# Kernel optimization log

Hardware: AMD Instinct MI355X
Metric: run time of the kernel (lower is better)

## Reference

```python
import jax, jax.numpy as jnp
import numpy as np

G, N, E, F_IN, F_OUT, C = 256, 512, 4096, 64, 64, 16


def setup_inputs() -> dict:
    key = jax.random.key(0)
    ks = jax.random.split(key, 6)
    x_batch = jax.random.normal(ks[0], (G, N, F_IN), dtype=jnp.float32)
    edge_index_batch = jax.random.randint(ks[1], (G, 2, E), 0, N, dtype=jnp.int32)
    conv_weight = jax.random.normal(ks[2], (F_OUT, F_IN), dtype=jnp.float32) * (1.0 / np.sqrt(F_IN))
    conv_bias = jax.random.normal(ks[3], (F_OUT,), dtype=jnp.float32) * 0.02
    lin_weight = jax.random.normal(ks[4], (C, F_OUT * N), dtype=jnp.float32) * (1.0 / np.sqrt(F_OUT * N))
    lin_bias = jax.random.normal(ks[5], (C,), dtype=jnp.float32) * 0.02
    return {"x_batch": x_batch, "edge_index_batch": edge_index_batch,
            "conv_weight": conv_weight, "conv_bias": conv_bias,
            "lin_weight": lin_weight, "lin_bias": lin_bias}


def _gcn_conv_graph(xw, edge_index, self_loops):
    # xw: [N, F_OUT] (already linearly transformed), edge_index: [2, E]
    row = jnp.concatenate([edge_index[0], self_loops])  # sources
    col = jnp.concatenate([edge_index[1], self_loops])  # targets
    ones = jnp.ones(row.shape[0], dtype=xw.dtype)
    deg = jax.ops.segment_sum(ones, col, num_segments=N)  # degree at target nodes
    dinv = jnp.where(deg > 0, jax.lax.rsqrt(deg), jnp.zeros_like(deg))
    norm = dinv[row] * dinv[col]                          # [E+N]
    msgs = xw[row] * norm[:, None]                        # gather + normalize
    return jax.ops.segment_sum(msgs, col, num_segments=N)  # scatter-add at targets


def reference(x_batch, edge_index_batch, conv_weight, conv_bias, lin_weight, lin_bias):
    # GCNConv (PyG defaults: self-loops, symmetric normalization, post-agg bias)
    xw = jnp.einsum('gnf,of->gno', x_batch, conv_weight)  # [G, N, F_OUT]
    self_loops = jnp.arange(N, dtype=edge_index_batch.dtype)
    h = jax.vmap(_gcn_conv_graph, in_axes=(0, 0, None))(xw, edge_index_batch, self_loops)
    h = h + conv_bias
    h = jax.nn.relu(h)
    flat = h.reshape(h.shape[0], -1)                      # [G, N*F_OUT]
    logits = flat @ lin_weight.T + lin_bias               # [G, C]
    return jax.nn.log_softmax(logits, axis=-1)
```

## Files before the change

kernel.cpp:

```cpp
#include <hip/hip_runtime.h>

#define Gn 256
#define Nn 512
#define En 4096
#define Fn 64
#define Cn 16
#define ET (En + Nn)

typedef _Float16 halfv8 __attribute__((ext_vector_type(8)));
typedef _Float16 halfv4 __attribute__((ext_vector_type(4)));
typedef _Float16 halfv2 __attribute__((ext_vector_type(2)));
typedef float    f32x4  __attribute__((ext_vector_type(4)));

__device__ __forceinline__ float pk_norm(unsigned p) {
    return (float)__builtin_bit_cast(_Float16, (unsigned short)(p & 0xffffu));
}

__global__ __launch_bounds__(1024, 4) void gcn_agg_conv(
    const float* __restrict__ x,
    const int*   __restrict__ ei,
    const float* __restrict__ w,
    const float* __restrict__ wbias,
    const float* __restrict__ lw,
    _Float16* __restrict__ hout,
    _Float16* __restrict__ lwh)
{
    __shared__ unsigned short xs_h[Nn * Fn];
    __shared__ unsigned short xhs[Nn * Fn];
    __shared__ unsigned short wts[Fn * Fn];
    __shared__ unsigned int   epk[ET + 8];
    __shared__ float dinv[Nn];
    __shared__ int   cnt[Nn];
    __shared__ int   wsum[8];

    const int g    = blockIdx.x;
    const int tid  = threadIdx.x;
    const int lane = tid & 63;
    const int wid  = tid >> 6;

    const float* xg = x + (size_t)g * Nn * Fn;
    const int*   es = ei + (size_t)g * 2 * En;
    const int*   ed = es + En;

    const int e0s = es[tid], e1s = es[tid + 1024], e2s = es[tid + 2048], e3s = es[tid + 3072];
    const int e0t = ed[tid], e1t = ed[tid + 1024], e2t = ed[tid + 2048], e3t = ed[tid + 3072];
    const float2 lv = *(const float2*)(lw + g * 2048 + tid * 2);
    const float4 wv = *(const float4*)(w + (tid >> 4) * Fn + (tid & 15) * 4);
    const int qq = (tid & 63) >> 4;
    float4 bv[4];
    #pragma unroll
    for (int to = 0; to < 4; ++to) bv[to] = *(const float4*)&wbias[to * 16 + qq * 4];
    float4 xv[8];
    #pragma unroll
    for (int it = 0; it < 8; ++it) xv[it] = *(const float4*)(xg + (tid + it * 1024) * 4);

    if (tid < Nn) dinv[tid] = 1.0f;
    __syncthreads();

    atomicAdd(&dinv[e0t], 1.0f);
    atomicAdd(&dinv[e1t], 1.0f);
    atomicAdd(&dinv[e2t], 1.0f);
    atomicAdd(&dinv[e3t], 1.0f);
    __syncthreads();

    int c = 0;
    if (tid < Nn) { float d = dinv[tid]; c = (int)d; dinv[tid] = rsqrtf(d); }
    int v_ = c;
    #pragma unroll
    for (int off = 1; off < 64; off <<= 1) {
        int u = __shfl_up(v_, off, 64);
        if (lane >= off) v_ += u;
    }
    if (wid < 8 && lane == 63) wsum[wid] = v_;
    __syncthreads();
    if (tid == 0) { int a = 0; for (int i = 0; i < 8; ++i) { int t = wsum[i]; wsum[i] = a; a += t; } }
    __syncthreads();
    if (tid < Nn) cnt[tid] = v_ - c + wsum[wid];
    __syncthreads();

    {
        #define FILL_EDGE(ss, tt) { \
            float nrm = dinv[ss] * dinv[tt]; \
            int slot = atomicAdd(&cnt[tt], 1); \
            unsigned short nb = __builtin_bit_cast(unsigned short, (_Float16)nrm); \
            epk[slot] = ((unsigned)(ss) << 16) | nb; }
        FILL_EDGE(e0s, e0t)
        FILL_EDGE(e1s, e1t)
        FILL_EDGE(e2s, e2t)
        FILL_EDGE(e3s, e3t)
        #undef FILL_EDGE
        if (tid < Nn) {
            float dv = dinv[tid];
            float nrm = dv * dv;
            int slot = atomicAdd(&cnt[tid], 1);
            unsigned short nb = __builtin_bit_cast(unsigned short, (_Float16)nrm);
            epk[slot] = ((unsigned)tid << 16) | nb;
        }
    }

    {
        halfv2 hl; hl[0] = (_Float16)lv.x; hl[1] = (_Float16)lv.y;
        *(halfv2*)(lwh + (size_t)g * 2048 + tid * 2) = hl;
    }

    {
        int o = tid >> 4, f0 = (tid & 15) * 4;
        halfv4 hv; hv[0]=(_Float16)wv.x; hv[1]=(_Float16)wv.y;
                   hv[2]=(_Float16)wv.z; hv[3]=(_Float16)wv.w;
        int blk = f0 >> 3, hf = (f0 >> 2) & 1;
        *(halfv4*)((char*)wts + o * 128 + ((blk ^ (o & 7)) * 16) + hf * 8) = hv;
    }

    #pragma unroll
    for (int it = 0; it < 8; ++it) {
        int idx = tid + it * 1024;
        float4 v = xv[it];
        halfv4 hv; hv[0]=(_Float16)v.x; hv[1]=(_Float16)v.y;
                   hv[2]=(_Float16)v.z; hv[3]=(_Float16)v.w;
        *(halfv4*)((char*)xs_h + idx * 8) = hv;
    }
    __syncthreads();

    {
        const int qid = lane >> 4, fl = lane & 15;
        for (int r = 0; r < 8; ++r) {
            int t = r * 64 + wid * 4 + qid;
            int beg = (t == 0) ? 0 : cnt[t - 1];
            int end = cnt[t];
            float a0 = 0.f, a1 = 0.f, a2 = 0.f, a3 = 0.f;
            unsigned pA0 = epk[beg],     pA1 = epk[beg + 1];
            unsigned pA2 = epk[beg + 2], pA3 = epk[beg + 3];
            int j = beg;
            for (; j + 4 <= end; j += 4) {
                unsigned pB0 = epk[j + 4], pB1 = epk[j + 5];
                unsigned pB2 = epk[j + 6], pB3 = epk[j + 7];
                int s0 = pA0 >> 16, s1 = pA1 >> 16, s2 = pA2 >> 16, s3 = pA3 >> 16;
                float n0 = pk_norm(pA0), n1 = pk_norm(pA1);
                float n2 = pk_norm(pA2), n3 = pk_norm(pA3);
                halfv4 x0 = *(const halfv4*)((const char*)xs_h + s0 * 128 + fl * 8);
                halfv4 x1 = *(const halfv4*)((const char*)xs_h + s1 * 128 + fl * 8);
                halfv4 x2 = *(const halfv4*)((const char*)xs_h + s2 * 128 + fl * 8);
                halfv4 x3 = *(const halfv4*)((const char*)xs_h + s3 * 128 + fl * 8);
                a0 += n0 * (float)x0[0] + n1 * (float)x1[0] + n2 * (float)x2[0] + n3 * (float)x3[0];
                a1 += n0 * (float)x0[1] + n1 * (float)x1[1] + n2 * (float)x2[1] + n3 * (float)x3[1];
                a2 += n0 * (float)x0[2] + n1 * (float)x1[2] + n2 * (float)x2[2] + n3 * (float)x3[2];
                a3 += n0 * (float)x0[3] + n1 * (float)x1[3] + n2 * (float)x2[3] + n3 * (float)x3[3];
                pA0 = pB0; pA1 = pB1; pA2 = pB2; pA3 = pB3;
            }
            for (; j < end; ++j) {
                int s = pA0 >> 16;
                float nm = pk_norm(pA0);
                halfv4 xvv = *(const halfv4*)((const char*)xs_h + s * 128 + fl * 8);
                a0 += nm * (float)xvv[0]; a1 += nm * (float)xvv[1];
                a2 += nm * (float)xvv[2]; a3 += nm * (float)xvv[3];
                pA0 = pA1; pA1 = pA2; pA2 = pA3;
            }
            halfv4 hv; hv[0]=(_Float16)a0; hv[1]=(_Float16)a1;
                       hv[2]=(_Float16)a2; hv[3]=(_Float16)a3;
            int dw = t * 32 + (((fl >> 1) ^ (t & 7)) * 4) + (fl & 1) * 2;
            *(halfv4*)((char*)xhs + dw * 4) = hv;
        }
    }
    __syncthreads();

    {
        const int m = lane & 15, q = lane >> 4;
        #pragma unroll
        for (int j = 0; j < 8; ++j) {
            int idx = wid * 8 + j, tm = idx >> 2, to = idx & 3;
            int n = tm * 16 + m, o = to * 16 + m;
            halfv8 X0 = *(const halfv8*)((const char*)xhs + n * 128 + ((q       ^ (n & 7)) * 16));
            halfv8 X1 = *(const halfv8*)((const char*)xhs + n * 128 + (((4 + q) ^ (n & 7)) * 16));
            halfv8 W0 = *(const halfv8*)((const char*)wts + o * 128 + ((q       ^ (o & 7)) * 16));
            halfv8 W1 = *(const halfv8*)((const char*)wts + o * 128 + (((4 + q) ^ (o & 7)) * 16));
            f32x4 acc = {0.f, 0.f, 0.f, 0.f};
            acc = __builtin_amdgcn_mfma_f32_16x16x32_f16(W0, X0, acc, 0, 0, 0);
            acc = __builtin_amdgcn_mfma_f32_16x16x32_f16(W1, X1, acc, 0, 0, 0);
            float4 bq = bv[j & 3];
            halfv4 hv;
            hv[0] = (_Float16)fmaxf(acc[0] + bq.x, 0.0f);
            hv[1] = (_Float16)fmaxf(acc[1] + bq.y, 0.0f);
            hv[2] = (_Float16)fmaxf(acc[2] + bq.z, 0.0f);
            hv[3] = (_Float16)fmaxf(acc[3] + bq.w, 0.0f);
            int sw = (to * 4 + q) ^ m;
            *(halfv4*)((char*)xs_h + n * 128 + sw * 8) = hv;
        }
    }
    __syncthreads();

    {
        _Float16* hg = hout + (size_t)g * (Nn * Fn);
        #pragma unroll
        for (int it = 0; it < 8; ++it) {
            int i = tid + it * 1024;
            int n = i >> 4, g64 = i & 15;
            uint2 vv = *(const uint2*)((const char*)xs_h + (n * 16 + (g64 ^ (n & 15))) * 8);
            *(uint2*)((char*)hg + (size_t)i * 8) = vv;
        }
    }
}

__global__ __launch_bounds__(256) void gcn_linear(
    const _Float16* __restrict__ h,
    const _Float16* __restrict__ lwh,
    float* __restrict__ part)
{
    __shared__ float red[4][64][4];
    const int cx = blockIdx.x;
    const int gy = blockIdx.y;
    const int tid = threadIdx.x, lane = tid & 63, wid = tid >> 6;
    const int ml = lane & 15, q = lane >> 4;

    const size_t kbase = (size_t)cx * 1024 + wid * 256;
    const _Float16* ha = h   + (size_t)(gy * 16 + ml) * (Nn * Fn) + kbase + q * 8;
    const _Float16* lb = lwh + (size_t)ml * (Nn * Fn) + kbase + q * 8;

    f32x4 acc = {0.f, 0.f, 0.f, 0.f};
    #pragma unroll
    for (int ks = 0; ks < 8; ++ks) {
        halfv8 a = *(const halfv8*)(ha + ks * 32);
        halfv8 b = *(const halfv8*)(lb + ks * 32);
        acc = __builtin_amdgcn_mfma_f32_16x16x32_f16(a, b, acc, 0, 0, 0);
    }
    #pragma unroll
    for (int r = 0; r < 4; ++r) red[wid][lane][r] = acc[r];
    __syncthreads();
    {
        int m = tid >> 4, cc = tid & 15;
        int sl = (m >> 2) * 16 + cc, rg = m & 3;
        float v = red[0][sl][rg] + red[1][sl][rg] + red[2][sl][rg] + red[3][sl][rg];
        part[(((size_t)(gy * 16 + m)) * 32 + cx) * Cn + cc] = v;
    }
}

__global__ __launch_bounds__(64) void gcn_softmax(
    const float* __restrict__ part,
    const float* __restrict__ lbias,
    float* __restrict__ out)
{
    const int g = blockIdx.x, lane = threadIdx.x;
    if (lane < Cn) {
        float v = lbias[lane];
        #pragma unroll
        for (int s = 0; s < 32; ++s) v += part[((size_t)g * 32 + s) * Cn + lane];
        float m = v;
        #pragma unroll
        for (int off = 8; off > 0; off >>= 1) m = fmaxf(m, __shfl_xor(m, off, 16));
        float ex = expf(v - m);
        float ssum = ex;
        #pragma unroll
        for (int off = 8; off > 0; off >>= 1) ssum += __shfl_xor(ssum, off, 16);
        out[g * Cn + lane] = v - m - logf(ssum);
    }
}

extern "C" void kernel_launch(void* const* d_in, const int* in_sizes, int n_in,
                              void* d_out, int out_size, void* d_ws, size_t ws_size,
                              hipStream_t stream) {
    const float* x  = (const float*)d_in[0];
    const int*   ei = (const int*)d_in[1];
    const float* w  = (const float*)d_in[2];
    const float* wb = (const float*)d_in[3];
    const float* lw = (const float*)d_in[4];
    const float* lb = (const float*)d_in[5];
    float* out = (float*)d_out;

    _Float16* hbuf = (_Float16*)d_ws;
    float* part = (float*)((char*)d_ws + (size_t)Gn * Nn * Fn * 2);
    _Float16* lwh = (_Float16*)((char*)d_ws + (size_t)Gn * Nn * Fn * 2
                                            + (size_t)Gn * 32 * Cn * 4);

    hipLaunchKernelGGL(gcn_agg_conv, dim3(Gn), dim3(1024), 0, stream,
                       x, ei, w, wb, lw, hbuf, lwh);
    hipLaunchKernelGGL(gcn_linear, dim3(32, 16), dim3(256), 0, stream,
                       hbuf, lwh, part);
    hipLaunchKernelGGL(gcn_softmax, dim3(Gn), dim3(64), 0, stream,
                       part, lb, out);
}
```

Baseline: 115.0 us.

## Fuse final linear layer and log-softmax into the per-graph GCN kernel

Instead of writing the fp16 hidden activations to global memory and running separate linear and softmax kernels, each graph's block now computes the 16 logits directly from shared memory. Each wavefront handles one class using fdot2 against an fp16 copy of the linear weights, then the block applies log-softmax. A small pre-kernel converts the linear weights to fp16, and the x loads are moved to overlap with the degree atomics. This removes the large intermediate global round-trip and two launches. In exchange, each block repeatedly streams the full 1 MB fp16 weight matrix, the per-block reduction is serialized, and register pressure changes.

```diff
diff --git a/kernel.cpp b/kernel.cpp
--- a/kernel.cpp
+++ b/kernel.cpp
@@ -16,14 +16,27 @@
     return (float)__builtin_bit_cast(_Float16, (unsigned short)(p & 0xffffu));
 }
 
-__global__ __launch_bounds__(1024, 4) void gcn_agg_conv(
+__global__ __launch_bounds__(256) void cvt_lw(
+    const float* __restrict__ lw,
+    _Float16* __restrict__ lwh)
+{
+    const int i = blockIdx.x * 256 + threadIdx.x;
+    float4 a = *((const float4*)lw + (size_t)i * 2);
+    float4 b = *((const float4*)lw + (size_t)i * 2 + 1);
+    halfv8 hv;
+    hv[0]=(_Float16)a.x; hv[1]=(_Float16)a.y; hv[2]=(_Float16)a.z; hv[3]=(_Float16)a.w;
+    hv[4]=(_Float16)b.x; hv[5]=(_Float16)b.y; hv[6]=(_Float16)b.z; hv[7]=(_Float16)b.w;
+    *(halfv8*)(lwh + (size_t)i * 8) = hv;
+}
+
+__global__ __launch_bounds__(1024, 4) void gcn_fused(
     const float* __restrict__ x,
     const int*   __restrict__ ei,
     const float* __restrict__ w,
     const float* __restrict__ wbias,
-    const float* __restrict__ lw,
-    _Float16* __restrict__ hout,
-    _Float16* __restrict__ lwh)
+    const _Float16* __restrict__ lwh,
+    const float* __restrict__ lbias,
+    float* __restrict__ out)
 {
     __shared__ unsigned short xs_h[Nn * Fn];
     __shared__ unsigned short xhs[Nn * Fn];
@@ -44,15 +57,6 @@
 
     const int e0s = es[tid], e1s = es[tid + 1024], e2s = es[tid + 2048], e3s = es[tid + 3072];
     const int e0t = ed[tid], e1t = ed[tid + 1024], e2t = ed[tid + 2048], e3t = ed[tid + 3072];
-    const float2 lv = *(const float2*)(lw + g * 2048 + tid * 2);
-    const float4 wv = *(const float4*)(w + (tid >> 4) * Fn + (tid & 15) * 4);
-    const int qq = (tid & 63) >> 4;
-    float4 bv[4];
-    #pragma unroll
-    for (int to = 0; to < 4; ++to) bv[to] = *(const float4*)&wbias[to * 16 + qq * 4];
-    float4 xv[8];
-    #pragma unroll
-    for (int it = 0; it < 8; ++it) xv[it] = *(const float4*)(xg + (tid + it * 1024) * 4);
 
     if (tid < Nn) dinv[tid] = 1.0f;
     __syncthreads();
@@ -61,6 +65,10 @@
     atomicAdd(&dinv[e1t], 1.0f);
     atomicAdd(&dinv[e2t], 1.0f);
     atomicAdd(&dinv[e3t], 1.0f);
+
+    float4 xv[8];
+    #pragma unroll
+    for (int it = 0; it < 8; ++it) xv[it] = *(const float4*)(xg + (tid + it * 1024) * 4);
     __syncthreads();
 
     int c = 0;
@@ -99,14 +107,10 @@
     }
 
     {
-        halfv2 hl; hl[0] = (_Float16)lv.x; hl[1] = (_Float16)lv.y;
-        *(halfv2*)(lwh + (size_t)g * 2048 + tid * 2) = hl;
-    }
-
-    {
         int o = tid >> 4, f0 = (tid & 15) * 4;
-        halfv4 hv; hv[0]=(_Float16)wv.x; hv[1]=(_Float16)wv.y;
-                   hv[2]=(_Float16)wv.z; hv[3]=(_Float16)wv.w;
+        float4 v = *(const float4*)(w + o * Fn + f0);
+        halfv4 hv; hv[0]=(_Float16)v.x; hv[1]=(_Float16)v.y;
+                   hv[2]=(_Float16)v.z; hv[3]=(_Float16)v.w;
         int blk = f0 >> 3, hf = (f0 >> 2) & 1;
         *(halfv4*)((char*)wts + o * 128 + ((blk ^ (o & 7)) * 16) + hf * 8) = hv;
     }
@@ -176,7 +180,7 @@
             f32x4 acc = {0.f, 0.f, 0.f, 0.f};
             acc = __builtin_amdgcn_mfma_f32_16x16x32_f16(W0, X0, acc, 0, 0, 0);
             acc = __builtin_amdgcn_mfma_f32_16x16x32_f16(W1, X1, acc, 0, 0, 0);
-            float4 bq = bv[j & 3];
+            float4 bq = *(const float4*)&wbias[to * 16 + q * 4];
             halfv4 hv;
             hv[0] = (_Float16)fmaxf(acc[0] + bq.x, 0.0f);
             hv[1] = (_Float16)fmaxf(acc[1] + bq.y, 0.0f);
@@ -189,60 +193,46 @@
     __syncthreads();
 
     {
-        _Float16* hg = hout + (size_t)g * (Nn * Fn);
-        #pragma unroll
-        for (int it = 0; it < 8; ++it) {
-            int i = tid + it * 1024;
-            int n = i >> 4, g64 = i & 15;
-            uint2 vv = *(const uint2*)((const char*)xs_h + (n * 16 + (g64 ^ (n & 15))) * 8);
-            *(uint2*)((char*)hg + (size_t)i * 8) = vv;
-        }
-    }
-}
-
-__global__ __launch_bounds__(256) void gcn_linear(
-    const _Float16* __restrict__ h,
-    const _Float16* __restrict__ lwh,
-    float* __restrict__ part)
-{
-    __shared__ float red[4][64][4];
-    const int cx = blockIdx.x;
-    const int gy = blockIdx.y;
-    const int tid = threadIdx.x, lane = tid & 63, wid = tid >> 6;
-    const int ml = lane & 15, q = lane >> 4;
-
-    const size_t kbase = (size_t)cx * 1024 + wid * 256;
-    const _Float16* ha = h   + (size_t)(gy * 16 + ml) * (Nn * Fn) + kbase + q * 8;
-    const _Float16* lb = lwh + (size_t)ml * (Nn * Fn) + kbase + q * 8;
-
-    f32x4 acc = {0.f, 0.f, 0.f, 0.f};
-    #pragma unroll
-    for (int ks = 0; ks < 8; ++ks) {
-        halfv8 a = *(const halfv8*)(ha + ks * 32);
-        halfv8 b = *(const halfv8*)(lb + ks * 32);
-        acc = __builtin_amdgcn_mfma_f32_16x16x32_f16(a, b, acc, 0, 0, 0);
-    }
-    #pragma unroll
-    for (int r = 0; r < 4; ++r) red[wid][lane][r] = acc[r];
-    __syncthreads();
-    {
-        int m = tid >> 4, cc = tid & 15;
-        int sl = (m >> 2) * 16 + cc, rg = m & 3;
-        float v = red[0][sl][rg] + red[1][sl][rg] + red[2][sl][rg] + red[3][sl][rg];
-        part[(((size_t)(gy * 16 + m)) * 32 + cx) * Cn + cc] = v;
-    }
-}
-
-__global__ __launch_bounds__(64) void gcn_softmax(
-    const float* __restrict__ part,
-    const float* __restrict__ lbias,
-    float* __restrict__ out)
-{
-    const int g = blockIdx.x, lane = threadIdx.x;
-    if (lane < Cn) {
-        float v = lbias[lane];
-        #pragma unroll
-        for (int s = 0; s < 32; ++s) v += part[((size_t)g * 32 + s) * Cn + lane];
+        const _Float16* lwc = lwh + (size_t)wid * (Nn * Fn);
+        const int l7 = lane & 7, l3 = lane >> 3;
+        float acc = 0.f;
+        #pragma unroll 4
+        for (int i = 0; i < 64; ++i) {
+            int n  = i * 8 + l3;
+            int rb = n << 7;
+            int sA = ((l7 * 2)     ^ (n & 15));
+            int sB = ((l7 * 2 + 1) ^ (n & 15));
+            halfv4 hA = *(const halfv4*)((const char*)xs_h + rb + sA * 8);
+            halfv4 hB = *(const halfv4*)((const char*)xs_h + rb + sB * 8);
+            halfv8 wv8 = *(const halfv8*)(lwc + (n << 6) + l7 * 8);
+#if __has_builtin(__builtin_amdgcn_fdot2)
+            halfv2 a0; a0[0]=hA[0]; a0[1]=hA[1];
+            halfv2 a1; a1[0]=hA[2]; a1[1]=hA[3];
+            halfv2 a2; a2[0]=hB[0]; a2[1]=hB[1];
+            halfv2 a3; a3[0]=hB[2]; a3[1]=hB[3];
+            halfv2 b0; b0[0]=wv8[0]; b0[1]=wv8[1];
+            halfv2 b1; b1[0]=wv8[2]; b1[1]=wv8[3];
+            halfv2 b2; b2[0]=wv8[4]; b2[1]=wv8[5];
+            halfv2 b3; b3[0]=wv8[6]; b3[1]=wv8[7];
+            acc = __builtin_amdgcn_fdot2(a0, b0, acc, false);
+            acc = __builtin_amdgcn_fdot2(a1, b1, acc, false);
+            acc = __builtin_amdgcn_fdot2(a2, b2, acc, false);
+            acc = __builtin_amdgcn_fdot2(a3, b3, acc, false);
+#else
+            acc += (float)hA[0]*(float)wv8[0] + (float)hA[1]*(float)wv8[1]
+                 + (float)hA[2]*(float)wv8[2] + (float)hA[3]*(float)wv8[3]
+                 + (float)hB[0]*(float)wv8[4] + (float)hB[1]*(float)wv8[5]
+                 + (float)hB[2]*(float)wv8[6] + (float)hB[3]*(float)wv8[7];
+#endif
+        }
+        #pragma unroll
+        for (int off = 32; off > 0; off >>= 1) acc += __shfl_xor(acc, off, 64);
+        if (lane == 0) dinv[wid] = acc;
+    }
+    __syncthreads();
+
+    if (tid < Cn) {
+        float v = dinv[tid] + lbias[tid];
         float m = v;
         #pragma unroll
         for (int off = 8; off > 0; off >>= 1) m = fmaxf(m, __shfl_xor(m, off, 16));
@@ -250,7 +240,7 @@
         float ssum = ex;
         #pragma unroll
         for (int off = 8; off > 0; off >>= 1) ssum += __shfl_xor(ssum, off, 16);
-        out[g * Cn + lane] = v - m - logf(ssum);
+        out[g * Cn + tid] = v - m - logf(ssum);
     }
 }
 
@@ -265,15 +255,9 @@
     const float* lb = (const float*)d_in[5];
     float* out = (float*)d_out;
 
-    _Float16* hbuf = (_Float16*)d_ws;
-    float* part = (float*)((char*)d_ws + (size_t)Gn * Nn * Fn * 2);
-    _Float16* lwh = (_Float16*)((char*)d_ws + (size_t)Gn * Nn * Fn * 2
-                                            + (size_t)Gn * 32 * Cn * 4);
-
-    hipLaunchKernelGGL(gcn_agg_conv, dim3(Gn), dim3(1024), 0, stream,
-                       x, ei, w, wb, lw, hbuf, lwh);
-    hipLaunchKernelGGL(gcn_linear, dim3(32, 16), dim3(256), 0, stream,
-                       hbuf, lwh, part);
-    hipLaunchKernelGGL(gcn_softmax, dim3(Gn), dim3(64), 0, stream,
-                       part, lb, out);
-}
+    _Float16* lwh = (_Float16*)d_ws;
+
+    hipLaunchKernelGGL(cvt_lw, dim3(256), dim3(256), 0, stream, lw, lwh);
+    hipLaunchKernelGGL(gcn_fused, dim3(Gn), dim3(1024), 0, stream,
+                       x, ei, w, wb, lwh, lb, out);
+}
```

New measurement: 112.6 us (median of 2 runs). 2.1% less time.
